# Optimization experiments

Hardware: AMD Instinct MI355X
Metric: run time of the kernel (lower is better)

The kernel has to match this reference:

```python
import jax, jax.numpy as jnp
import numpy as np

CLASSES = 21
IOU_THRESH = 0.5
ALPHA, GAMMA = 0.25, 2.0
CLS_W, REG_W = 1.0, 1.0


def _make_boxes(key, shape):
    # valid xyxy boxes: x1<x2, y1<y2 inside unit square
    k1, k2 = jax.random.split(key)
    xy1 = jax.random.uniform(k1, shape[:-1] + (2,)) * 0.8
    wh = jax.random.uniform(k2, shape[:-1] + (2,)) * 0.19 + 0.01
    return jnp.concatenate([xy1, xy1 + wh], axis=-1).astype(jnp.float32)


def setup_inputs() -> dict:
    key = jax.random.key(0)
    k1, k2, k3, k4, k5 = jax.random.split(key, 5)
    B, A, T = 4, 49152, 50
    return {
        "classification_preds": jax.random.normal(k1, (B, A, CLASSES), dtype=jnp.float32),
        "boxes_preds": _make_boxes(k2, (B, A, 4)),
        "anchors": _make_boxes(k3, (B, A, 4)),
        "target_boxes": _make_boxes(k4, (B, T, 4)),
        "target_labels": jax.random.randint(k5, (B, T), 1, CLASSES),  # 1..20 (0=background)
    }


def compute_iou(a, b):
    # a: [T,4] xyxy, b: [A,4] xyxy -> [T,A]
    lt = jnp.maximum(a[:, None, :2], b[None, :, :2])
    rb = jnp.minimum(a[:, None, 2:], b[None, :, 2:])
    wh = jnp.clip(rb - lt, 0.0)
    inter = wh[..., 0] * wh[..., 1]
    area_a = (a[:, 2] - a[:, 0]) * (a[:, 3] - a[:, 1])
    area_b = (b[:, 2] - b[:, 0]) * (b[:, 3] - b[:, 1])
    union = area_a[:, None] + area_b[None, :] - inter
    return inter / jnp.clip(union, 1e-8)


def encode(boxes, anchors):
    # xyxy -> center offsets relative to anchors
    bc = (boxes[:, :2] + boxes[:, 2:]) * 0.5
    bwh = boxes[:, 2:] - boxes[:, :2]
    ac = (anchors[:, :2] + anchors[:, 2:]) * 0.5
    awh = anchors[:, 2:] - anchors[:, :2]
    txy = (bc - ac) / awh
    twh = jnp.log(bwh / awh)
    return jnp.concatenate([txy, twh], axis=-1)


def focal_loss(logits, targets):
    p = jax.nn.sigmoid(logits)
    ce = -(targets * jax.nn.log_sigmoid(logits) + (1.0 - targets) * jax.nn.log_sigmoid(-logits))
    pt = targets * p + (1.0 - targets) * (1.0 - p)
    alpha_t = targets * ALPHA + (1.0 - targets) * (1.0 - ALPHA)
    return alpha_t * (1.0 - pt) ** GAMMA * ce


def smooth_l1(x, y):
    d = jnp.abs(x - y)
    return jnp.where(d < 1.0, 0.5 * d * d, d - 0.5)


def reference(classification_preds, boxes_preds, anchors, target_boxes, target_labels):
    cls = classification_preds.reshape(-1, CLASSES)   # [A, C]
    box = boxes_preds.reshape(-1, 4)                  # [A, 4]
    anc = anchors.reshape(-1, 4)                      # [A, 4]
    tb = target_boxes.reshape(-1, 4)                  # [T, 4]
    tl = target_labels.reshape(-1)                    # [T]

    iou = compute_iou(tb, anc)                        # [T, A]
    max_iou = jnp.max(iou, axis=0)                    # [A]
    tid = jnp.argmax(iou, axis=0)                     # [A]
    pos = max_iou >= IOU_THRESH                       # [A]
    pos_cnt = jnp.sum(pos.astype(jnp.int32))
    norm = jnp.clip(pos_cnt, 1).astype(cls.dtype)

    onehot = jax.nn.one_hot(tl[tid], CLASSES, dtype=cls.dtype)        # [A, C]
    background = jax.nn.one_hot(0, CLASSES, dtype=cls.dtype)          # [C]
    cls_tgt = jnp.where(pos[:, None], onehot, background[None, :])    # [A, C]

    cls_loss = jnp.sum(focal_loss(cls, cls_tgt)) / norm

    enc_pred = encode(box, anc)                       # [A, 4]
    enc_tgt = encode(tb[tid], anc)                    # [A, 4]
    reg_elem = smooth_l1(enc_pred, enc_tgt) * pos[:, None].astype(cls.dtype)
    reg_loss = jnp.sum(reg_elem) / (norm * 4.0)       # mean over positive elements
    reg_loss = jnp.where(pos_cnt > 0, reg_loss, 0.0)

    wc = cls_loss * CLS_W
    wr = reg_loss * REG_W
    return (wc + wr, wc, wr)
```

## Files before the change

kernel.cpp:

```cpp
#include <hip/hip_runtime.h>
#include <hip/hip_bf16.h>


#define CLASSES 21
#define TPB 256

__global__ void zero_kernel(float* __restrict__ accums) {
    if (threadIdx.x < 3) accums[threadIdx.x] = 0.0f;
}

__global__ __launch_bounds__(TPB)
void main_kernel(const float* __restrict__ cls,
                 const float4* __restrict__ box,
                 const float4* __restrict__ anc,
                 const int* __restrict__ labels,
                 const float4* __restrict__ tbox,
                 float* __restrict__ accums,
                 int A, int T) {
    int a = blockIdx.x * blockDim.x + threadIdx.x;

    float cls_p = 0.0f, reg_p = 0.0f, pos_p = 0.0f;

    if (a < A) {
        float4 av = anc[a];
        float ax1 = av.x, ay1 = av.y, ax2 = av.z, ay2 = av.w;
        float areaA = (ax2 - ax1) * (ay2 - ay1);

        float bI = 0.0f, bU = 1.0f;
        int bT = 0;
        #pragma unroll 4
        for (int t = 0; t < T; ++t) {
            float4 tv = tbox[t];
            float ta = (tv.z - tv.x) * (tv.w - tv.y);
            float lx = fmaxf(tv.x, ax1);
            float ly = fmaxf(tv.y, ay1);
            float rx = fminf(tv.z, ax2);
            float ry = fminf(tv.w, ay2);
            float w = fmaxf(rx - lx, 0.0f);
            float h = fmaxf(ry - ly, 0.0f);
            float inter = w * h;
            float uni = ta + areaA - inter;
            bool gt = inter * bU > bI * uni;
            bI = gt ? inter : bI;
            bU = gt ? uni : bU;
            bT = gt ? t : bT;
        }
        bool pos = (bI + bI) >= bU;

        int hot = pos ? labels[bT] : 0;
        const float* crow = cls + (size_t)a * CLASSES;
        float csum = 0.0f;
        #pragma unroll
        for (int j = 0; j < CLASSES; ++j) {
            float x = crow[j];
            float y = (j == hot) ? -x : x;
            float em = __expf(-fabsf(y));
            float sp = fmaxf(y, 0.0f) + __logf(1.0f + em);
            float r1 = __builtin_amdgcn_rcpf(1.0f + em);
            float sg = (y >= 0.0f) ? r1 : em * r1;
            float f = sg * sg * sp;
            csum = fmaf(f, (j == hot) ? (1.0f / 3.0f) : 1.0f, csum);
        }
        cls_p = csum * 0.75f;

        if (pos) {
            pos_p = 1.0f;
            float4 bv = box[a];
            float4 tv = tbox[bT];
            float aw = ax2 - ax1, ah = ay2 - ay1;
            float acx = (ax1 + ax2) * 0.5f, acy = (ay1 + ay2) * 0.5f;
            float ep0 = ((bv.x + bv.z) * 0.5f - acx) / aw;
            float ep1 = ((bv.y + bv.w) * 0.5f - acy) / ah;
            float ep2 = __logf((bv.z - bv.x) / aw);
            float ep3 = __logf((bv.w - bv.y) / ah);
            float et0 = ((tv.x + tv.z) * 0.5f - acx) / aw;
            float et1 = ((tv.y + tv.w) * 0.5f - acy) / ah;
            float et2 = __logf((tv.z - tv.x) / aw);
            float et3 = __logf((tv.w - tv.y) / ah);
            float r = 0.0f, d;
            d = fabsf(ep0 - et0); r += (d < 1.0f) ? 0.5f * d * d : d - 0.5f;
            d = fabsf(ep1 - et1); r += (d < 1.0f) ? 0.5f * d * d : d - 0.5f;
            d = fabsf(ep2 - et2); r += (d < 1.0f) ? 0.5f * d * d : d - 0.5f;
            d = fabsf(ep3 - et3); r += (d < 1.0f) ? 0.5f * d * d : d - 0.5f;
            reg_p = r;
        }
    }

    #pragma unroll
    for (int off = 32; off > 0; off >>= 1) {
        cls_p += __shfl_down(cls_p, off, 64);
        reg_p += __shfl_down(reg_p, off, 64);
        pos_p += __shfl_down(pos_p, off, 64);
    }
    __shared__ float red[3][TPB / 64];
    int wave = threadIdx.x >> 6;
    int lane = threadIdx.x & 63;
    if (lane == 0) {
        red[0][wave] = cls_p;
        red[1][wave] = reg_p;
        red[2][wave] = pos_p;
    }
    __syncthreads();
    if (threadIdx.x == 0) {
        float c = 0.0f, r = 0.0f, p = 0.0f;
        #pragma unroll
        for (int wv = 0; wv < TPB / 64; ++wv) {
            c += red[0][wv]; r += red[1][wv]; p += red[2][wv];
        }
        atomicAdd(&accums[0], c);
        atomicAdd(&accums[1], r);
        atomicAdd(&accums[2], p);
    }
}

__global__ void fin_kernel(const float* __restrict__ accums,
                           float* __restrict__ out) {
    float cls_sum = accums[0];
    float reg_sum = accums[1];
    float cnt = accums[2];
    float norm = fmaxf(cnt, 1.0f);
    float wc = cls_sum / norm;
    float wr = (cnt > 0.0f) ? reg_sum / (norm * 4.0f) : 0.0f;
    out[0] = wc + wr;
    out[1] = wc;
    out[2] = wr;
}

extern "C" void kernel_launch(void* const* d_in, const int* in_sizes, int n_in,
                              void* d_out, int out_size, void* d_ws, size_t ws_size,
                              hipStream_t stream) {
    const float* cls  = (const float*)d_in[0];
    const float4* box = (const float4*)d_in[1];
    const float4* anc = (const float4*)d_in[2];
    const float4* tb  = (const float4*)d_in[3];
    const int* tl     = (const int*)d_in[4];

    int A = in_sizes[0] / CLASSES;
    int T = in_sizes[4];

    float* accums = (float*)d_ws;

    zero_kernel<<<1, 64, 0, stream>>>(accums);

    int main_blocks = (A + TPB - 1) / TPB;
    main_kernel<<<main_blocks, TPB, 0, stream>>>(cls, box, anc, tl, tb,
                                                 accums, A, T);

    fin_kernel<<<1, 1, 0, stream>>>(accums, (float*)d_out);
}
```

Baseline: 123.4 us.

## Split each anchor across four lanes and replace atomics with per-block partials

Each anchor is now handled by four threads, each scanning a quarter of the targets from shared memory. The per-lane results are merged with a packed IoU/index key through lane shuffles, and the class-loss work is split across the same four lanes. The global atomics and the zero kernel are replaced by per-block partial sums that a parallel final kernel reduces, which removes one launch. The argmax tie-breaking now works on a truncated IoU key with an approximate reciprocal, and targets are capped at 256 by the shared buffer and the 8-bit index, so chosen targets and positive decisions can differ slightly from the reference.

```diff
diff --git a/kernel.cpp b/kernel.cpp
--- a/kernel.cpp
+++ b/kernel.cpp
@@ -4,10 +4,8 @@
 
 #define CLASSES 21
 #define TPB 256
-
-__global__ void zero_kernel(float* __restrict__ accums) {
-    if (threadIdx.x < 3) accums[threadIdx.x] = 0.0f;
-}
+#define APB 64
+#define MAXT 256
 
 __global__ __launch_bounds__(TPB)
 void main_kernel(const float* __restrict__ cls,
@@ -15,23 +13,37 @@
                  const float4* __restrict__ anc,
                  const int* __restrict__ labels,
                  const float4* __restrict__ tbox,
-                 float* __restrict__ accums,
+                 float* __restrict__ pc,
+                 float* __restrict__ pr,
+                 float* __restrict__ pp,
                  int A, int T) {
-    int a = blockIdx.x * blockDim.x + threadIdx.x;
+    __shared__ float4 s_tb[MAXT];
+    __shared__ float  s_ta[MAXT];
+
+    int tid = threadIdx.x;
+    for (int t = tid; t < T; t += TPB) {
+        float4 v = tbox[t];
+        s_tb[t] = v;
+        s_ta[t] = (v.z - v.x) * (v.w - v.y);
+    }
+    __syncthreads();
+
+    int p = tid & 3;
+    int a = blockIdx.x * APB + (tid >> 2);
 
     float cls_p = 0.0f, reg_p = 0.0f, pos_p = 0.0f;
+    float ax1 = 0.f, ay1 = 0.f, ax2 = 0.f, ay2 = 0.f;
+    float bIou = 0.0f;
+    int bKey = 0;
 
     if (a < A) {
         float4 av = anc[a];
-        float ax1 = av.x, ay1 = av.y, ax2 = av.z, ay2 = av.w;
+        ax1 = av.x; ay1 = av.y; ax2 = av.z; ay2 = av.w;
         float areaA = (ax2 - ax1) * (ay2 - ay1);
 
-        float bI = 0.0f, bU = 1.0f;
-        int bT = 0;
-        #pragma unroll 4
-        for (int t = 0; t < T; ++t) {
-            float4 tv = tbox[t];
-            float ta = (tv.z - tv.x) * (tv.w - tv.y);
+        for (int t = p; t < T; t += 4) {
+            float4 tv = s_tb[t];
+            float ta = s_ta[t];
             float lx = fmaxf(tv.x, ax1);
             float ly = fmaxf(tv.y, ay1);
             float rx = fminf(tv.z, ax2);
@@ -39,34 +51,46 @@
             float w = fmaxf(rx - lx, 0.0f);
             float h = fmaxf(ry - ly, 0.0f);
             float inter = w * h;
-            float uni = ta + areaA - inter;
-            bool gt = inter * bU > bI * uni;
-            bI = gt ? inter : bI;
-            bU = gt ? uni : bU;
-            bT = gt ? t : bT;
+            float uni = (ta + areaA) - inter;
+            float iou = inter * __builtin_amdgcn_rcpf(uni);
+            bIou = fmaxf(bIou, iou);
+            int key = (__float_as_int(iou) & 0xFFFFFF00) | (255 - t);
+            bKey = max(bKey, key);
         }
-        bool pos = (bI + bI) >= bU;
+    }
+
+    bKey = max(bKey, __shfl_xor(bKey, 1, 64));
+    bKey = max(bKey, __shfl_xor(bKey, 2, 64));
+    bIou = fmaxf(bIou, __shfl_xor(bIou, 1, 64));
+    bIou = fmaxf(bIou, __shfl_xor(bIou, 2, 64));
+
+    if (a < A) {
+        int bT = 255 - (bKey & 0xFF);
+        bool pos = bIou >= 0.5f;
 
         int hot = pos ? labels[bT] : 0;
         const float* crow = cls + (size_t)a * CLASSES;
         float csum = 0.0f;
         #pragma unroll
-        for (int j = 0; j < CLASSES; ++j) {
-            float x = crow[j];
-            float y = (j == hot) ? -x : x;
-            float em = __expf(-fabsf(y));
-            float sp = fmaxf(y, 0.0f) + __logf(1.0f + em);
-            float r1 = __builtin_amdgcn_rcpf(1.0f + em);
-            float sg = (y >= 0.0f) ? r1 : em * r1;
-            float f = sg * sg * sp;
-            csum = fmaf(f, (j == hot) ? (1.0f / 3.0f) : 1.0f, csum);
+        for (int k = 0; k < 6; ++k) {
+            int j = p + 4 * k;
+            if (j < CLASSES) {
+                float x = crow[j];
+                float y = (j == hot) ? -x : x;
+                float em = __expf(-fabsf(y));
+                float sp = fmaxf(y, 0.0f) + __logf(1.0f + em);
+                float r1 = __builtin_amdgcn_rcpf(1.0f + em);
+                float sg = (y >= 0.0f) ? r1 : em * r1;
+                float f = sg * sg * sp;
+                csum = fmaf(f, (j == hot) ? (1.0f / 3.0f) : 1.0f, csum);
+            }
         }
         cls_p = csum * 0.75f;
 
-        if (pos) {
+        if (pos && p == 0) {
             pos_p = 1.0f;
             float4 bv = box[a];
-            float4 tv = tbox[bT];
+            float4 tv = s_tb[bT];
             float aw = ax2 - ax1, ah = ay2 - ay1;
             float acx = (ax1 + ax2) * 0.5f, acy = (ay1 + ay2) * 0.5f;
             float ep0 = ((bv.x + bv.z) * 0.5f - acx) / aw;
@@ -93,37 +117,60 @@
         pos_p += __shfl_down(pos_p, off, 64);
     }
     __shared__ float red[3][TPB / 64];
-    int wave = threadIdx.x >> 6;
-    int lane = threadIdx.x & 63;
+    int wave = tid >> 6;
+    int lane = tid & 63;
     if (lane == 0) {
         red[0][wave] = cls_p;
         red[1][wave] = reg_p;
         red[2][wave] = pos_p;
     }
     __syncthreads();
-    if (threadIdx.x == 0) {
-        float c = 0.0f, r = 0.0f, p = 0.0f;
+    if (tid == 0) {
+        float c = 0.0f, r = 0.0f, q = 0.0f;
         #pragma unroll
         for (int wv = 0; wv < TPB / 64; ++wv) {
-            c += red[0][wv]; r += red[1][wv]; p += red[2][wv];
+            c += red[0][wv]; r += red[1][wv]; q += red[2][wv];
         }
-        atomicAdd(&accums[0], c);
-        atomicAdd(&accums[1], r);
-        atomicAdd(&accums[2], p);
+        pc[blockIdx.x] = c;
+        pr[blockIdx.x] = r;
+        pp[blockIdx.x] = q;
     }
 }
 
-__global__ void fin_kernel(const float* __restrict__ accums,
-                           float* __restrict__ out) {
-    float cls_sum = accums[0];
-    float reg_sum = accums[1];
-    float cnt = accums[2];
-    float norm = fmaxf(cnt, 1.0f);
-    float wc = cls_sum / norm;
-    float wr = (cnt > 0.0f) ? reg_sum / (norm * 4.0f) : 0.0f;
-    out[0] = wc + wr;
-    out[1] = wc;
-    out[2] = wr;
+__global__ __launch_bounds__(TPB)
+void fin_kernel(const float* __restrict__ pc,
+                const float* __restrict__ pr,
+                const float* __restrict__ pp,
+                int nb, float* __restrict__ out) {
+    int tid = threadIdx.x;
+    float c = 0.0f, r = 0.0f, q = 0.0f;
+    for (int i = tid; i < nb; i += TPB) {
+        c += pc[i]; r += pr[i]; q += pp[i];
+    }
+    #pragma unroll
+    for (int off = 32; off > 0; off >>= 1) {
+        c += __shfl_down(c, off, 64);
+        r += __shfl_down(r, off, 64);
+        q += __shfl_down(q, off, 64);
+    }
+    __shared__ float red[3][TPB / 64];
+    int wave = tid >> 6;
+    int lane = tid & 63;
+    if (lane == 0) { red[0][wave] = c; red[1][wave] = r; red[2][wave] = q; }
+    __syncthreads();
+    if (tid == 0) {
+        float cs = 0.0f, rs = 0.0f, qs = 0.0f;
+        #pragma unroll
+        for (int wv = 0; wv < TPB / 64; ++wv) {
+            cs += red[0][wv]; rs += red[1][wv]; qs += red[2][wv];
+        }
+        float norm = fmaxf(qs, 1.0f);
+        float wc = cs / norm;
+        float wr = (qs > 0.0f) ? rs / (norm * 4.0f) : 0.0f;
+        out[0] = wc + wr;
+        out[1] = wc;
+        out[2] = wr;
+    }
 }
 
 extern "C" void kernel_launch(void* const* d_in, const int* in_sizes, int n_in,
@@ -138,13 +185,11 @@
     int A = in_sizes[0] / CLASSES;
     int T = in_sizes[4];
 
-    float* accums = (float*)d_ws;
+    int nb = (A + APB - 1) / APB;
+    float* pc = (float*)d_ws;
+    float* pr = pc + nb;
+    float* pp = pr + nb;
 
-    zero_kernel<<<1, 64, 0, stream>>>(accums);
-
-    int main_blocks = (A + TPB - 1) / TPB;
-    main_kernel<<<main_blocks, TPB, 0, stream>>>(cls, box, anc, tl, tb,
-                                                 accums, A, T);
-
-    fin_kernel<<<1, 1, 0, stream>>>(accums, (float*)d_out);
+    main_kernel<<<nb, TPB, 0, stream>>>(cls, box, anc, tl, tb, pc, pr, pp, A, T);
+    fin_kernel<<<1, TPB, 0, stream>>>(pc, pr, pp, nb, (float*)d_out);
 }
```

Measured after the change: 106.4 us. 1.16x faster.
